# Kernel tuning notes

Measured on AMD Instinct MI355X. Metric: run time of the kernel, lower is better.

The kernel has to match this reference:

```python
import jax, jax.numpy as jnp
import numpy as np

DIM = 1024
N_HEADS = 16
HEAD_DIM = DIM // N_HEADS
LORA_DIM = 16
B, T = 4, 1024


def _rope(x):
    # x: [B, H, T, D] with D even; rotate first/second halves (torch impl style)
    D = x.shape[-1]
    half = D // 2
    theta = 1.0 / (10000.0 ** (jnp.arange(0, D, 2, dtype=jnp.float32) / D))  # [D/2]
    pos = jnp.arange(x.shape[-2], dtype=jnp.float32)                         # [T]
    pt = pos[:, None] * theta[None, :]                                       # [T, D/2]
    sin, cos = jnp.sin(pt), jnp.cos(pt)
    xr, xi = x[..., :half], x[..., half:]
    return jnp.concatenate([xr * cos - xi * sin, xr * sin + xi * cos], axis=-1)


def setup_inputs() -> dict:
    key = jax.random.key(0)
    ks = jax.random.split(key, 16)
    def n(k, shape, std=0.02):
        return jax.random.normal(k, shape, jnp.float32) * std
    return {
        "x": jax.random.normal(ks[0], (B, T, DIM), jnp.float32),
        "q_w": n(ks[1], (DIM, DIM)),
        "k_w": n(ks[2], (DIM, DIM)),
        "v_w": n(ks[3], (DIM, DIM)),
        "q_a": n(ks[4], (LORA_DIM, DIM), 0.001),
        "q_b": n(ks[5], (DIM, LORA_DIM), 0.001),
        "q_l": jax.random.normal(ks[6], (DIM,), jnp.float32),
        "k_a": n(ks[7], (LORA_DIM, DIM), 0.001),
        "k_b": n(ks[8], (DIM, LORA_DIM), 0.001),
        "k_l": jax.random.normal(ks[9], (DIM,), jnp.float32),
        "v_a": n(ks[10], (LORA_DIM, DIM), 0.001),
        "v_b": n(ks[11], (DIM, LORA_DIM), 0.001),
        "v_l": jax.random.normal(ks[12], (DIM,), jnp.float32),
        "proj_w": n(ks[13], (DIM, DIM)),
        "proj_b": n(ks[14], (DIM,)),
    }


def reference(x, q_w, k_w, v_w, q_a, q_b, q_l, k_a, k_b, k_l,
              v_a, v_b, v_l, proj_w, proj_b):
    Bb, Tt, C = x.shape
    # token shift: xx[t] = x[t-1], xx[0] = 0 (ZeroPad2d((0,0,1,-1)))
    xx = jnp.pad(x, ((0, 0), (1, 0), (0, 0)))[:, :Tt]
    xxx = xx - x

    def lora(a, b, lam):
        return lam + jnp.tanh(x @ a.T) @ b.T  # [B,T,C]

    q = (x + xxx * lora(q_a, q_b, q_l)) @ q_w.T
    k = (x + xxx * lora(k_a, k_b, k_l)) @ k_w.T
    v = (x + xxx * lora(v_a, v_b, v_l)) @ v_w.T

    def split_heads(t):
        return t.reshape(Bb, Tt, N_HEADS, HEAD_DIM).transpose(0, 2, 1, 3)  # [B,H,T,D]

    q = _rope(split_heads(q))
    k = _rope(split_heads(k))
    v = split_heads(v)

    scale = 1.0 / np.sqrt(HEAD_DIM).astype(np.float32)
    scores = jnp.einsum('bhqd,bhkd->bhqk', q, k) * scale
    causal = jnp.tril(jnp.ones((Tt, Tt), dtype=bool))
    scores = jnp.where(causal, scores, jnp.float32(-1e30))
    att = jax.nn.softmax(scores, axis=-1)
    out = jnp.einsum('bhqk,bhkd->bhqd', att, v)
    out = out.transpose(0, 2, 1, 3).reshape(Bb, Tt, C)
    return out @ proj_w.T + proj_b
```

## Files before the change

kernel.cpp:

```cpp
#include <hip/hip_runtime.h>
#include <hip/hip_bf16.h>

typedef __hip_bfloat16 bf16;
typedef __attribute__((ext_vector_type(8))) short bf16x8;
typedef __attribute__((ext_vector_type(4))) float f32x4;

typedef const __attribute__((address_space(1))) unsigned int* gp_t;
typedef __attribute__((address_space(3))) unsigned int* lp_t;

__device__ __forceinline__ bf16 tobf(float f) { return __float2bfloat16(f); }
__device__ __forceinline__ float tof(bf16 h) { return __bfloat162float(h); }

__device__ __forceinline__ short bfbits(float f) {
    bf16 h = __float2bfloat16(f);
    return *reinterpret_cast<short*>(&h);
}
__device__ __forceinline__ bf16x8 pack8(float4 a, float4 b) {
    bf16x8 r;
    r[0] = bfbits(a.x); r[1] = bfbits(a.y); r[2] = bfbits(a.z); r[3] = bfbits(a.w);
    r[4] = bfbits(b.x); r[5] = bfbits(b.y); r[6] = bfbits(b.z); r[7] = bfbits(b.w);
    return r;
}

__device__ __forceinline__ void gload_lds16(const void* g, void* l) {
    __builtin_amdgcn_global_load_lds((gp_t)g, (lp_t)l, 16, 0, 0);
}

__global__ __launch_bounds__(256) void convert_w(const float* qw, const float* kw,
                                                 const float* vw, const float* pw,
                                                 bf16* dst) {
    int m = blockIdx.y;
    const float* src = m == 0 ? qw : (m == 1 ? kw : (m == 2 ? vw : pw));
    bf16* d = dst + (size_t)m * (1u << 20);
    int i = (blockIdx.x * 256 + threadIdx.x) * 4;
    float4 f = *(const float4*)(src + i);
    d[i + 0] = tobf(f.x);
    d[i + 1] = tobf(f.y);
    d[i + 2] = tobf(f.z);
    d[i + 3] = tobf(f.w);
}

__global__ __launch_bounds__(256) void lora_gate_fused(
    const float* x,
    const float* qa, const float* ka, const float* va,
    const float* qbw, const float* ql,
    const float* kbw, const float* kl,
    const float* vbw, const float* vl,
    bf16* xqo, bf16* xko, bf16* xvo) {
    const int XS = 1028;
    int row0 = blockIdx.x * 16;
    int t0 = row0 & 1023;
    int tid = threadIdx.x;
    int wave = tid >> 6, lane = tid & 63;
    int quad = lane >> 4, l16 = lane & 15;

    __shared__ float sx[17 * 1028];
    __shared__ float sT[16 * 48];

    {
        int prow = (row0 == 0) ? 0 : row0 - 1;
        for (int i = 0; i < 17; ++i) {
            int grow = (i == 0) ? prow : row0 + i - 1;
            gload_lds16(x + (size_t)grow * 1024 + wave * 256 + lane * 4,
                        &sx[i * XS + wave * 256]);
        }
    }
    __syncthreads();

    if (wave < 3) {
        const float* am = wave == 0 ? qa : (wave == 1 ? ka : va);
        f32x4 acc = (f32x4){0.f, 0.f, 0.f, 0.f};
#pragma unroll 4
        for (int k0 = 0; k0 < 1024; k0 += 32) {
            const float* xs = &sx[(1 + l16) * XS + k0 + quad * 8];
            bf16x8 af = pack8(*(const float4*)xs, *(const float4*)(xs + 4));
            const float* as = am + (size_t)l16 * 1024 + k0 + quad * 8;
            bf16x8 bf_ = pack8(*(const float4*)as, *(const float4*)(as + 4));
            acc = __builtin_amdgcn_mfma_f32_16x16x32_bf16(af, bf_, acc, 0, 0, 0);
        }
#pragma unroll
        for (int r = 0; r < 4; ++r)
            sT[(quad * 4 + r) * 48 + wave * 16 + l16] = tanhf(acc[r]);
    }
    __syncthreads();

#pragma unroll
    for (int u = 0; u < 4; ++u) {
        int d = tid + u * 256;
        float qbv[16], kbv[16], vbv[16];
#pragma unroll
        for (int p = 0; p < 4; ++p) {
            *(float4*)&qbv[p * 4] = *(const float4*)(qbw + (size_t)d * 16 + p * 4);
            *(float4*)&kbv[p * 4] = *(const float4*)(kbw + (size_t)d * 16 + p * 4);
            *(float4*)&vbv[p * 4] = *(const float4*)(vbw + (size_t)d * 16 + p * 4);
        }
        float qlv = ql[d], klv = kl[d], vlv = vl[d];
        float xp = (t0 == 0) ? 0.f : sx[0 * XS + d];
        for (int rr = 0; rr < 16; ++rr) {
            float xc = sx[(rr + 1) * XS + d];
            float dx = xp - xc;
            float gq = qlv, gk = klv, gv = vlv;
#pragma unroll
            for (int j = 0; j < 16; ++j) {
                gq += sT[rr * 48 + j] * qbv[j];
                gk += sT[rr * 48 + 16 + j] * kbv[j];
                gv += sT[rr * 48 + 32 + j] * vbv[j];
            }
            size_t o = (size_t)(row0 + rr) * 1024 + d;
            xqo[o] = tobf(xc + dx * gq);
            xko[o] = tobf(xc + dx * gk);
            xvo[o] = tobf(xc + dx * gv);
            xp = xc;
        }
    }
}

__global__ __launch_bounds__(256) void gemm128(
    const bf16* A0, const bf16* A1, const bf16* A2,
    const bf16* W0, const bf16* W1, const bf16* W2,
    bf16* C0, bf16* C1, bf16* C2,
    const float* bias, float* outF, int proj, int zcnt) {
    const int K = 1024;
    int ppx = (zcnt * 32) >> 3;
    int xcd = blockIdx.x & 7;
    int j = blockIdx.x >> 3;
    int pair = xcd * ppx + (j >> 3);
    int n0 = (j & 7) * 128;
    int bz = pair >> 5;
    int m0 = (pair & 31) * 128;

    const bf16* A = bz == 0 ? A0 : (bz == 1 ? A1 : A2);
    const bf16* W = bz == 0 ? W0 : (bz == 1 ? W1 : W2);
    bf16* C = bz == 0 ? C0 : (bz == 1 ? C1 : C2);

    __shared__ alignas(16) bf16 sA[64 * 64];
    __shared__ alignas(16) bf16 sB[64 * 64];

    int wave = threadIdx.x >> 6, lane = threadIdx.x & 63;
    int quad = lane >> 4, l16 = lane & 15;

    f32x4 acc[4][4];
#pragma unroll
    for (int i = 0; i < 4; i++)
#pragma unroll
        for (int j2 = 0; j2 < 4; j2++) acc[i][j2] = (f32x4){0.f, 0.f, 0.f, 0.f};

    int Rb0 = wave * 16 + (lane >> 3);
    int s0 = lane & 7;

    auto stage = [&](int k0) {
#pragma unroll
        for (int p = 0; p < 2; p++) {
            int R = Rb0 + p * 8;
            int cs = s0 ^ (R & 7);
            int mr = 2 * R + (cs >> 2);
            int kc = (cs & 3) * 8;
            gload_lds16(A + (size_t)(m0 + mr) * K + k0 + kc, &sA[(wave * 16 + p * 8) * 64]);
            gload_lds16(W + (size_t)(n0 + mr) * K + k0 + kc, &sB[(wave * 16 + p * 8) * 64]);
        }
    };

    int mw = (wave >> 1) * 64, nw = (wave & 1) * 64;
    int slot = (((l16 & 1) << 2) | quad) ^ ((l16 >> 1) & 7);
    int abase = ((mw >> 1) + (l16 >> 1)) * 64 + slot * 8;
    int bbase = ((nw >> 1) + (l16 >> 1)) * 64 + slot * 8;

    for (int it = 0; it < 32; ++it) {
        __syncthreads();
        stage(it * 32);
        __syncthreads();
        bf16x8 af[4], bfr[4];
#pragma unroll
        for (int f = 0; f < 4; f++) {
            af[f] = *(const bf16x8*)&sA[abase + f * 512];
            bfr[f] = *(const bf16x8*)&sB[bbase + f * 512];
        }
#pragma unroll
        for (int i = 0; i < 4; i++)
#pragma unroll
            for (int j2 = 0; j2 < 4; j2++)
                acc[i][j2] = __builtin_amdgcn_mfma_f32_16x16x32_bf16(af[i], bfr[j2], acc[i][j2], 0, 0, 0);
    }

    if (proj) {
#pragma unroll
        for (int i = 0; i < 4; i++) {
            int mrow = m0 + mw + i * 16 + quad * 4;
#pragma unroll
            for (int j2 = 0; j2 < 4; j2++) {
                int col = n0 + nw + j2 * 16 + l16;
                float bv = bias[col];
#pragma unroll
                for (int r = 0; r < 4; r++)
                    outF[(size_t)(mrow + r) * 1024 + col] = acc[i][j2][r] + bv;
            }
        }
    } else if (bz < 2) {
        float sc = (bz == 0) ? 0.125f : 1.0f;
        int tb = ((m0 + mw) & 1023) + quad * 4;
#pragma unroll
        for (int j2 = 0; j2 < 2; j2++) {
            int d = j2 * 16 + l16;
            float theta = __expf(-(float)d * (9.210340371976184f / 32.0f));
            float s1, c1, s16, c16, st, ct;
            sincosf(theta, &s1, &c1);
            sincosf(16.0f * theta, &s16, &c16);
            sincosf((float)tb * theta, &st, &ct);
            int col = n0 + nw + j2 * 16 + l16;
#pragma unroll
            for (int i = 0; i < 4; i++) {
                int mrow = m0 + mw + i * 16 + quad * 4;
                float c = ct, s = st;
#pragma unroll
                for (int r = 0; r < 4; r++) {
                    float xr = acc[i][j2][r], xi = acc[i][j2 + 2][r];
                    C[(size_t)(mrow + r) * 1024 + col] = tobf((xr * c - xi * s) * sc);
                    C[(size_t)(mrow + r) * 1024 + col + 32] = tobf((xr * s + xi * c) * sc);
                    float cn = c * c1 - s * s1;
                    s = s * c1 + c * s1;
                    c = cn;
                }
                float cn = ct * c16 - st * s16;
                st = st * c16 + ct * s16;
                ct = cn;
            }
        }
    } else {
#pragma unroll
        for (int i = 0; i < 4; i++) {
            int mrow = m0 + mw + i * 16 + quad * 4;
#pragma unroll
            for (int j2 = 0; j2 < 4; j2++) {
                int col = n0 + nw + j2 * 16 + l16;
#pragma unroll
                for (int r = 0; r < 4; r++)
                    C[(size_t)(mrow + r) * 1024 + col] = tobf(acc[i][j2][r]);
            }
        }
    }
}

__global__ __launch_bounds__(256) void v_transpose(const bf16* v, bf16* Vt) {
    int bh = blockIdx.x, tblk = blockIdx.y;
    int b = bh >> 4, h = bh & 15;
    int t0 = tblk * 64;
    int tid = threadIdx.x;

    __shared__ bf16 sv[64 * 65];
    {
        int r = tid >> 2;
        int c0 = (tid & 3) * 16;
        size_t g = ((size_t)(b * 1024 + t0 + r)) * 1024 + h * 64 + c0;
#pragma unroll
        for (int u = 0; u < 16; u++) sv[(c0 + u) * 65 + r] = v[g + u];
    }
    __syncthreads();
    {
        int d = tid >> 2;
        int tc = (tid & 3) * 16;
        size_t g = ((size_t)(bh * 64 + d)) * 1024 + t0 + tc;
#pragma unroll
        for (int u = 0; u < 16; u++) Vt[g + u] = sv[d * 65 + tc + u];
    }
}

__global__ __launch_bounds__(256) void attention(const bf16* Qm, const bf16* Km,
                                                 const bf16* Vt, bf16* attn) {
    int gid = blockIdx.x;
    int qblk = 15 - (gid >> 6);
    int bh = (((gid >> 3) & 7) << 3) | (gid & 7);
    int b = bh >> 4, h = bh & 15;
    int wave = threadIdx.x >> 6, lane = threadIdx.x & 63;
    int quad = lane >> 4, l16 = lane & 15;
    int m7 = l16 & 7;

    const bf16* Qb = Qm + (size_t)b * 1024 * 1024 + h * 64;
    const bf16* Kb = Km + (size_t)b * 1024 * 1024 + h * 64;
    const bf16* Vb = Vt + (size_t)bh * 64 * 1024;

    __shared__ alignas(16) bf16 sK[2][64 * 64];
    __shared__ alignas(16) bf16 sV[2][64 * 64];
    __shared__ alignas(16) bf16 sP[4][16 * 64];

    int srow = lane >> 3;
    int scol = ((lane & 7) ^ srow) * 8;

    auto stage = [&](int kt, int bufi) {
#pragma unroll
        for (int p = 0; p < 2; p++) {
            int rbase = p * 32 + wave * 8;
            gload_lds16(Kb + (size_t)(kt * 64 + rbase + srow) * 1024 + scol, &sK[bufi][rbase * 64]);
            gload_lds16(Vb + (size_t)(rbase + srow) * 1024 + kt * 64 + scol, &sV[bufi][rbase * 64]);
        }
    };

    int qrow0 = qblk * 64 + wave * 16;
    bf16x8 aq0 = *(const bf16x8*)&Qb[(size_t)(qrow0 + l16) * 1024 + quad * 8];
    bf16x8 aq1 = *(const bf16x8*)&Qb[(size_t)(qrow0 + l16) * 1024 + quad * 8 + 32];

    f32x4 o[4];
#pragma unroll
    for (int nt = 0; nt < 4; nt++) o[nt] = (f32x4){0.f, 0.f, 0.f, 0.f};
    float mrow[4], lrow[4];
#pragma unroll
    for (int r = 0; r < 4; r++) { mrow[r] = -3.0e38f; lrow[r] = 0.f; }

    stage(0, 0);

    int buf = 0;
    for (int kt = 0; kt <= qblk; ++kt, buf ^= 1) {
        __syncthreads();
        if (kt < qblk) stage(kt + 1, buf ^ 1);

        f32x4 S[4];
#pragma unroll
        for (int j = 0; j < 4; j++) {
            int row = j * 16 + l16;
            bf16x8 bk0 = *(const bf16x8*)&sK[buf][row * 64 + ((quad ^ m7) * 8)];
            bf16x8 bk1 = *(const bf16x8*)&sK[buf][row * 64 + (((quad + 4) ^ m7) * 8)];
            f32x4 z = __builtin_amdgcn_mfma_f32_16x16x32_bf16(aq0, bk0, (f32x4){0.f, 0.f, 0.f, 0.f}, 0, 0, 0);
            S[j] = __builtin_amdgcn_mfma_f32_16x16x32_bf16(aq1, bk1, z, 0, 0, 0);
        }
        if (kt == qblk) {
#pragma unroll
            for (int j = 0; j < 4; j++) {
                int key = kt * 64 + j * 16 + l16;
#pragma unroll
                for (int r = 0; r < 4; r++) {
                    int qr = qrow0 + quad * 4 + r;
                    if (key > qr) S[j][r] = -3.0e38f;
                }
            }
        }
        float alpha[4];
#pragma unroll
        for (int r = 0; r < 4; r++) {
            float vmax = fmaxf(fmaxf(S[0][r], S[1][r]), fmaxf(S[2][r], S[3][r]));
            vmax = fmaxf(vmax, __shfl_xor(vmax, 1));
            vmax = fmaxf(vmax, __shfl_xor(vmax, 2));
            vmax = fmaxf(vmax, __shfl_xor(vmax, 4));
            vmax = fmaxf(vmax, __shfl_xor(vmax, 8));
            float mn = fmaxf(mrow[r], vmax);
            alpha[r] = __expf(mrow[r] - mn);
            mrow[r] = mn;
        }
        float rs[4] = {0.f, 0.f, 0.f, 0.f};
#pragma unroll
        for (int j = 0; j < 4; j++)
#pragma unroll
            for (int r = 0; r < 4; r++) {
                float p = __expf(S[j][r] - mrow[r]);
                S[j][r] = p;
                rs[r] += p;
            }
#pragma unroll
        for (int r = 0; r < 4; r++) {
            float v = rs[r];
            v += __shfl_xor(v, 1);
            v += __shfl_xor(v, 2);
            v += __shfl_xor(v, 4);
            v += __shfl_xor(v, 8);
            lrow[r] = lrow[r] * alpha[r] + v;
        }
#pragma unroll
        for (int nt = 0; nt < 4; nt++)
#pragma unroll
            for (int r = 0; r < 4; r++) o[nt][r] *= alpha[r];

#pragma unroll
        for (int j = 0; j < 4; j++) {
            int c = j * 2 + (l16 >> 3);
#pragma unroll
            for (int r = 0; r < 4; r++) {
                int prow = quad * 4 + r;
                sP[wave][prow * 64 + ((c ^ (prow & 7)) * 8) + m7] = tobf(S[j][r]);
            }
        }
        asm volatile("s_waitcnt lgkmcnt(0)" ::: "memory");
        bf16x8 ap0 = *(const bf16x8*)&sP[wave][l16 * 64 + ((quad ^ m7) * 8)];
        bf16x8 ap1 = *(const bf16x8*)&sP[wave][l16 * 64 + (((quad + 4) ^ m7) * 8)];
#pragma unroll
        for (int nt = 0; nt < 4; nt++) {
            int row = nt * 16 + l16;
            bf16x8 bv0 = *(const bf16x8*)&sV[buf][row * 64 + ((quad ^ m7) * 8)];
            bf16x8 bv1 = *(const bf16x8*)&sV[buf][row * 64 + (((quad + 4) ^ m7) * 8)];
            o[nt] = __builtin_amdgcn_mfma_f32_16x16x32_bf16(ap0, bv0, o[nt], 0, 0, 0);
            o[nt] = __builtin_amdgcn_mfma_f32_16x16x32_bf16(ap1, bv1, o[nt], 0, 0, 0);
        }
    }

    float invl[4];
#pragma unroll
    for (int r = 0; r < 4; r++) invl[r] = 1.0f / lrow[r];
#pragma unroll
    for (int nt = 0; nt < 4; nt++)
#pragma unroll
        for (int r = 0; r < 4; r++) {
            int t = qrow0 + quad * 4 + r;
            int col = h * 64 + nt * 16 + l16;
            attn[(size_t)(b * 1024 + t) * 1024 + col] = tobf(o[nt][r] * invl[r]);
        }
}

extern "C" void kernel_launch(void* const* d_in, const int* in_sizes, int n_in,
                              void* d_out, int out_size, void* d_ws, size_t ws_size,
                              hipStream_t stream) {
    const float* x = (const float*)d_in[0];
    const float* qw = (const float*)d_in[1];
    const float* kw = (const float*)d_in[2];
    const float* vw = (const float*)d_in[3];
    const float* qa = (const float*)d_in[4];
    const float* qb = (const float*)d_in[5];
    const float* ql = (const float*)d_in[6];
    const float* ka = (const float*)d_in[7];
    const float* kb = (const float*)d_in[8];
    const float* kl = (const float*)d_in[9];
    const float* va = (const float*)d_in[10];
    const float* vb = (const float*)d_in[11];
    const float* vl = (const float*)d_in[12];
    const float* pw = (const float*)d_in[13];
    const float* pb = (const float*)d_in[14];
    float* out = (float*)d_out;

    char* ws = (char*)d_ws;
    const size_t MB = 1024 * 1024;
    bf16* wqb = (bf16*)ws;
    bf16* wkb = wqb + 1048576;
    bf16* wvb = wkb + 1048576;
    bf16* wpb = wvb + 1048576;
    bf16* xqb = (bf16*)(ws + 8 * MB);
    bf16* xkb = xqb + 4194304;
    bf16* xvb = xkb + 4194304;
    bf16* qm = (bf16*)(ws + 32 * MB);
    bf16* km = qm + 4194304;
    bf16* vm = km + 4194304;
    bf16* Vt = xvb;
    bf16* attn = xqb;

    convert_w<<<dim3(1024, 4), 256, 0, stream>>>(qw, kw, vw, pw, wqb);
    lora_gate_fused<<<256, 256, 0, stream>>>(x, qa, ka, va, qb, ql, kb, kl, vb, vl,
                                             xqb, xkb, xvb);
    gemm128<<<768, 256, 0, stream>>>(xqb, xkb, xvb, wqb, wkb, wvb, qm, km, vm,
                                     nullptr, nullptr, 0, 3);
    v_transpose<<<dim3(64, 16), 256, 0, stream>>>(vm, Vt);
    attention<<<1024, 256, 0, stream>>>(qm, km, Vt, attn);
    gemm128<<<256, 256, 0, stream>>>(attn, nullptr, nullptr, wpb, nullptr, nullptr,
                                     nullptr, nullptr, nullptr, pb, out, 1, 1);
}
```

Baseline: 221.1 us.

## Fuse weight conversion into LoRA kernel and process two query tiles per attention block

Removes the separate weight-conversion launch by folding the fp32-to-bf16 weight conversion into the LoRA gate kernel, where each of the 256 blocks converts a 16K-element slice. The attention kernel now handles 128 query rows per block (two 64-row halves) so each staged K/V tile is reused by both halves, halving the grid to 512 blocks and cutting K/V global traffic. In exchange there are more registers per thread, fewer blocks to fill the GPU, and the causal load is paired differently, which may leave blocks less balanced.

```diff
diff --git a/kernel.cpp b/kernel.cpp
--- a/kernel.cpp
+++ b/kernel.cpp
@@ -24,20 +24,6 @@
 
 __device__ __forceinline__ void gload_lds16(const void* g, void* l) {
     __builtin_amdgcn_global_load_lds((gp_t)g, (lp_t)l, 16, 0, 0);
-}
-
-__global__ __launch_bounds__(256) void convert_w(const float* qw, const float* kw,
-                                                 const float* vw, const float* pw,
-                                                 bf16* dst) {
-    int m = blockIdx.y;
-    const float* src = m == 0 ? qw : (m == 1 ? kw : (m == 2 ? vw : pw));
-    bf16* d = dst + (size_t)m * (1u << 20);
-    int i = (blockIdx.x * 256 + threadIdx.x) * 4;
-    float4 f = *(const float4*)(src + i);
-    d[i + 0] = tobf(f.x);
-    d[i + 1] = tobf(f.y);
-    d[i + 2] = tobf(f.z);
-    d[i + 3] = tobf(f.w);
 }
 
 __global__ __launch_bounds__(256) void lora_gate_fused(
@@ -46,6 +32,8 @@
     const float* qbw, const float* ql,
     const float* kbw, const float* kl,
     const float* vbw, const float* vl,
+    const float* qw, const float* kw, const float* vw, const float* pw,
+    bf16* wdst,
     bf16* xqo, bf16* xko, bf16* xvo) {
     const int XS = 1028;
     int row0 = blockIdx.x * 16;
@@ -63,6 +51,23 @@
             int grow = (i == 0) ? prow : row0 + i - 1;
             gload_lds16(x + (size_t)grow * 1024 + wave * 256 + lane * 4,
                         &sx[i * XS + wave * 256]);
+        }
+    }
+    {
+        int m = blockIdx.x >> 6;
+        const float* src = m == 0 ? qw : (m == 1 ? kw : (m == 2 ? vw : pw));
+        bf16* dst = wdst + (size_t)m * (1u << 20);
+        int off = (blockIdx.x & 63) * 16384;
+#pragma unroll
+        for (int u = 0; u < 16; ++u) {
+            int i = off + u * 1024 + tid * 4;
+            float4 f = *(const float4*)(src + i);
+            ushort4 o4;
+            o4.x = (unsigned short)bfbits(f.x);
+            o4.y = (unsigned short)bfbits(f.y);
+            o4.z = (unsigned short)bfbits(f.z);
+            o4.w = (unsigned short)bfbits(f.w);
+            *(ushort4*)&dst[i] = o4;
         }
     }
     __syncthreads();
@@ -267,7 +272,7 @@
 __global__ __launch_bounds__(256) void attention(const bf16* Qm, const bf16* Km,
                                                  const bf16* Vt, bf16* attn) {
     int gid = blockIdx.x;
-    int qblk = 15 - (gid >> 6);
+    int q0 = 7 - (gid >> 6);
     int bh = (((gid >> 3) & 7) << 3) | (gid & 7);
     int b = bh >> 4, h = bh & 15;
     int wave = threadIdx.x >> 6, lane = threadIdx.x & 63;
@@ -294,112 +299,131 @@
         }
     };
 
-    int qrow0 = qblk * 64 + wave * 16;
-    bf16x8 aq0 = *(const bf16x8*)&Qb[(size_t)(qrow0 + l16) * 1024 + quad * 8];
-    bf16x8 aq1 = *(const bf16x8*)&Qb[(size_t)(qrow0 + l16) * 1024 + quad * 8 + 32];
-
-    f32x4 o[4];
-#pragma unroll
-    for (int nt = 0; nt < 4; nt++) o[nt] = (f32x4){0.f, 0.f, 0.f, 0.f};
-    float mrow[4], lrow[4];
-#pragma unroll
-    for (int r = 0; r < 4; r++) { mrow[r] = -3.0e38f; lrow[r] = 0.f; }
-
+    int qr0[2];
+    qr0[0] = q0 * 128 + wave * 16;
+    qr0[1] = qr0[0] + 64;
+    bf16x8 aq[2][2];
+#pragma unroll
+    for (int qh = 0; qh < 2; qh++) {
+        aq[qh][0] = *(const bf16x8*)&Qb[(size_t)(qr0[qh] + l16) * 1024 + quad * 8];
+        aq[qh][1] = *(const bf16x8*)&Qb[(size_t)(qr0[qh] + l16) * 1024 + quad * 8 + 32];
+    }
+
+    f32x4 o[2][4];
+    float mrow[2][4], lrow[2][4];
+#pragma unroll
+    for (int qh = 0; qh < 2; qh++)
+#pragma unroll
+        for (int r = 0; r < 4; r++) {
+            o[qh][r] = (f32x4){0.f, 0.f, 0.f, 0.f};
+            mrow[qh][r] = -3.0e38f;
+            lrow[qh][r] = 0.f;
+        }
+
+    int ntiles = 2 * q0 + 2;
     stage(0, 0);
 
     int buf = 0;
-    for (int kt = 0; kt <= qblk; ++kt, buf ^= 1) {
+    for (int kt = 0; kt < ntiles; ++kt, buf ^= 1) {
         __syncthreads();
-        if (kt < qblk) stage(kt + 1, buf ^ 1);
-
-        f32x4 S[4];
-#pragma unroll
-        for (int j = 0; j < 4; j++) {
-            int row = j * 16 + l16;
-            bf16x8 bk0 = *(const bf16x8*)&sK[buf][row * 64 + ((quad ^ m7) * 8)];
-            bf16x8 bk1 = *(const bf16x8*)&sK[buf][row * 64 + (((quad + 4) ^ m7) * 8)];
-            f32x4 z = __builtin_amdgcn_mfma_f32_16x16x32_bf16(aq0, bk0, (f32x4){0.f, 0.f, 0.f, 0.f}, 0, 0, 0);
-            S[j] = __builtin_amdgcn_mfma_f32_16x16x32_bf16(aq1, bk1, z, 0, 0, 0);
-        }
-        if (kt == qblk) {
+        if (kt + 1 < ntiles) stage(kt + 1, buf ^ 1);
+
+#pragma unroll
+        for (int qh = 0; qh < 2; qh++) {
+            if (kt > 2 * q0 + qh) continue;
+
+            f32x4 S[4];
 #pragma unroll
             for (int j = 0; j < 4; j++) {
-                int key = kt * 64 + j * 16 + l16;
+                int row = j * 16 + l16;
+                bf16x8 bk0 = *(const bf16x8*)&sK[buf][row * 64 + ((quad ^ m7) * 8)];
+                bf16x8 bk1 = *(const bf16x8*)&sK[buf][row * 64 + (((quad + 4) ^ m7) * 8)];
+                f32x4 z = __builtin_amdgcn_mfma_f32_16x16x32_bf16(aq[qh][0], bk0, (f32x4){0.f, 0.f, 0.f, 0.f}, 0, 0, 0);
+                S[j] = __builtin_amdgcn_mfma_f32_16x16x32_bf16(aq[qh][1], bk1, z, 0, 0, 0);
+            }
+            if (kt == 2 * q0 + qh) {
+#pragma unroll
+                for (int j = 0; j < 4; j++) {
+                    int key = kt * 64 + j * 16 + l16;
+#pragma unroll
+                    for (int r = 0; r < 4; r++) {
+                        int qr = qr0[qh] + quad * 4 + r;
+                        if (key > qr) S[j][r] = -3.0e38f;
+                    }
+                }
+            }
+            float alpha[4];
+#pragma unroll
+            for (int r = 0; r < 4; r++) {
+                float vmax = fmaxf(fmaxf(S[0][r], S[1][r]), fmaxf(S[2][r], S[3][r]));
+                vmax = fmaxf(vmax, __shfl_xor(vmax, 1));
+                vmax = fmaxf(vmax, __shfl_xor(vmax, 2));
+                vmax = fmaxf(vmax, __shfl_xor(vmax, 4));
+                vmax = fmaxf(vmax, __shfl_xor(vmax, 8));
+                float mn = fmaxf(mrow[qh][r], vmax);
+                alpha[r] = __expf(mrow[qh][r] - mn);
+                mrow[qh][r] = mn;
+            }
+            float rs[4] = {0.f, 0.f, 0.f, 0.f};
+#pragma unroll
+            for (int j = 0; j < 4; j++)
 #pragma unroll
                 for (int r = 0; r < 4; r++) {
-                    int qr = qrow0 + quad * 4 + r;
-                    if (key > qr) S[j][r] = -3.0e38f;
+                    float p = __expf(S[j][r] - mrow[qh][r]);
+                    S[j][r] = p;
+                    rs[r] += p;
                 }
-            }
-        }
-        float alpha[4];
-#pragma unroll
-        for (int r = 0; r < 4; r++) {
-            float vmax = fmaxf(fmaxf(S[0][r], S[1][r]), fmaxf(S[2][r], S[3][r]));
-            vmax = fmaxf(vmax, __shfl_xor(vmax, 1));
-            vmax = fmaxf(vmax, __shfl_xor(vmax, 2));
-            vmax = fmaxf(vmax, __shfl_xor(vmax, 4));
-            vmax = fmaxf(vmax, __shfl_xor(vmax, 8));
-            float mn = fmaxf(mrow[r], vmax);
-            alpha[r] = __expf(mrow[r] - mn);
-            mrow[r] = mn;
-        }
-        float rs[4] = {0.f, 0.f, 0.f, 0.f};
-#pragma unroll
-        for (int j = 0; j < 4; j++)
 #pragma unroll
             for (int r = 0; r < 4; r++) {
-                float p = __expf(S[j][r] - mrow[r]);
-                S[j][r] = p;
-                rs[r] += p;
-            }
-#pragma unroll
-        for (int r = 0; r < 4; r++) {
-            float v = rs[r];
-            v += __shfl_xor(v, 1);
-            v += __shfl_xor(v, 2);
-            v += __shfl_xor(v, 4);
-            v += __shfl_xor(v, 8);
-            lrow[r] = lrow[r] * alpha[r] + v;
-        }
+                float v = rs[r];
+                v += __shfl_xor(v, 1);
+                v += __shfl_xor(v, 2);
+                v += __shfl_xor(v, 4);
+                v += __shfl_xor(v, 8);
+                lrow[qh][r] = lrow[qh][r] * alpha[r] + v;
+            }
+#pragma unroll
+            for (int nt = 0; nt < 4; nt++)
+#pragma unroll
+                for (int r = 0; r < 4; r++) o[qh][nt][r] *= alpha[r];
+
+#pragma unroll
+            for (int j = 0; j < 4; j++) {
+                int c = j * 2 + (l16 >> 3);
+#pragma unroll
+                for (int r = 0; r < 4; r++) {
+                    int prow = quad * 4 + r;
+                    sP[wave][prow * 64 + ((c ^ (prow & 7)) * 8) + m7] = tobf(S[j][r]);
+                }
+            }
+            asm volatile("s_waitcnt lgkmcnt(0)" ::: "memory");
+            bf16x8 ap0 = *(const bf16x8*)&sP[wave][l16 * 64 + ((quad ^ m7) * 8)];
+            bf16x8 ap1 = *(const bf16x8*)&sP[wave][l16 * 64 + (((quad + 4) ^ m7) * 8)];
+#pragma unroll
+            for (int nt = 0; nt < 4; nt++) {
+                int row = nt * 16 + l16;
+                bf16x8 bv0 = *(const bf16x8*)&sV[buf][row * 64 + ((quad ^ m7) * 8)];
+                bf16x8 bv1 = *(const bf16x8*)&sV[buf][row * 64 + (((quad + 4) ^ m7) * 8)];
+                o[qh][nt] = __builtin_amdgcn_mfma_f32_16x16x32_bf16(ap0, bv0, o[qh][nt], 0, 0, 0);
+                o[qh][nt] = __builtin_amdgcn_mfma_f32_16x16x32_bf16(ap1, bv1, o[qh][nt], 0, 0, 0);
+            }
+        }
+    }
+
+#pragma unroll
+    for (int qh = 0; qh < 2; qh++) {
+        float invl[4];
+#pragma unroll
+        for (int r = 0; r < 4; r++) invl[r] = 1.0f / lrow[qh][r];
 #pragma unroll
         for (int nt = 0; nt < 4; nt++)
 #pragma unroll
-            for (int r = 0; r < 4; r++) o[nt][r] *= alpha[r];
-
-#pragma unroll
-        for (int j = 0; j < 4; j++) {
-            int c = j * 2 + (l16 >> 3);
-#pragma unroll
             for (int r = 0; r < 4; r++) {
-                int prow = quad * 4 + r;
-                sP[wave][prow * 64 + ((c ^ (prow & 7)) * 8) + m7] = tobf(S[j][r]);
-            }
-        }
-        asm volatile("s_waitcnt lgkmcnt(0)" ::: "memory");
-        bf16x8 ap0 = *(const bf16x8*)&sP[wave][l16 * 64 + ((quad ^ m7) * 8)];
-        bf16x8 ap1 = *(const bf16x8*)&sP[wave][l16 * 64 + (((quad + 4) ^ m7) * 8)];
-#pragma unroll
-        for (int nt = 0; nt < 4; nt++) {
-            int row = nt * 16 + l16;
-            bf16x8 bv0 = *(const bf16x8*)&sV[buf][row * 64 + ((quad ^ m7) * 8)];
-            bf16x8 bv1 = *(const bf16x8*)&sV[buf][row * 64 + (((quad + 4) ^ m7) * 8)];
-            o[nt] = __builtin_amdgcn_mfma_f32_16x16x32_bf16(ap0, bv0, o[nt], 0, 0, 0);
-            o[nt] = __builtin_amdgcn_mfma_f32_16x16x32_bf16(ap1, bv1, o[nt], 0, 0, 0);
-        }
-    }
-
-    float invl[4];
-#pragma unroll
-    for (int r = 0; r < 4; r++) invl[r] = 1.0f / lrow[r];
-#pragma unroll
-    for (int nt = 0; nt < 4; nt++)
-#pragma unroll
-        for (int r = 0; r < 4; r++) {
-            int t = qrow0 + quad * 4 + r;
-            int col = h * 64 + nt * 16 + l16;
-            attn[(size_t)(b * 1024 + t) * 1024 + col] = tobf(o[nt][r] * invl[r]);
-        }
+                int t = qr0[qh] + quad * 4 + r;
+                int col = h * 64 + nt * 16 + l16;
+                attn[(size_t)(b * 1024 + t) * 1024 + col] = tobf(o[qh][nt][r] * invl[r]);
+            }
+    }
 }
 
 extern "C" void kernel_launch(void* const* d_in, const int* in_sizes, int n_in,
@@ -437,13 +461,13 @@
     bf16* Vt = xvb;
     bf16* attn = xqb;
 
-    convert_w<<<dim3(1024, 4), 256, 0, stream>>>(qw, kw, vw, pw, wqb);
     lora_gate_fused<<<256, 256, 0, stream>>>(x, qa, ka, va, qb, ql, kb, kl, vb, vl,
+                                             qw, kw, vw, pw, wqb,
                                              xqb, xkb, xvb);
     gemm128<<<768, 256, 0, stream>>>(xqb, xkb, xvb, wqb, wkb, wvb, qm, km, vm,
                                      nullptr, nullptr, 0, 3);
     v_transpose<<<dim3(64, 16), 256, 0, stream>>>(vm, Vt);
-    attention<<<1024, 256, 0, stream>>>(qm, km, Vt, attn);
+    attention<<<512, 256, 0, stream>>>(qm, km, Vt, attn);
     gemm128<<<256, 256, 0, stream>>>(attn, nullptr, nullptr, wpb, nullptr, nullptr,
                                      nullptr, nullptr, nullptr, pb, out, 1, 1);
 }
```

New measurement: 235.7 us. 1.07x slower.
